# Optimization experiments

Hardware: AMD Instinct MI355X
Metric: run time of the kernel (lower is better)

## Reference

```python
import jax, jax.numpy as jnp
import numpy as np

N = 50000   # nodes
E = 800000  # edges
D = 128     # nfeat == nhid
C = 40      # nclass
L = 4       # nlayer
EPS_BN = 1e-5
EPS_PN = 1e-6
PN_SCALE = 1.0


def setup_inputs() -> dict:
    key = jax.random.key(0)
    ks = jax.random.split(key, 10)
    x = jax.random.normal(ks[0], (N, D), jnp.float32)
    edge_row = jax.random.randint(ks[1], (E,), 0, N)   # destination rows of adj
    edge_col = jax.random.randint(ks[2], (E,), 0, N)   # source cols of adj
    edge_val = jax.random.uniform(ks[3], (E,), jnp.float32)
    # BatchNorm1d(nfeat) affine params
    bn_gamma = jnp.ones((D,), jnp.float32)
    bn_beta = jnp.zeros((D,), jnp.float32)
    s = 1.0 / np.sqrt(D)
    fc_in_w = jax.random.uniform(ks[4], (D, D), jnp.float32, -s, s)
    fc_in_b = jax.random.uniform(ks[5], (D,), jnp.float32, -s, s)
    gc_w = jax.random.uniform(ks[6], (L, D, D), jnp.float32, -s, s)
    gc_b = jax.random.uniform(ks[7], (L, D), jnp.float32, -s, s)
    fc_out_w = jax.random.uniform(ks[8], (D, C), jnp.float32, -s, s)
    fc_out_b = jax.random.uniform(ks[9], (C,), jnp.float32, -s, s)
    return dict(x=x, edge_row=edge_row, edge_col=edge_col, edge_val=edge_val,
                bn_gamma=bn_gamma, bn_beta=bn_beta,
                fc_in_w=fc_in_w, fc_in_b=fc_in_b,
                gc_w=gc_w, gc_b=gc_b,
                fc_out_w=fc_out_w, fc_out_b=fc_out_b)


def pair_norm(x):
    # PairNorm 'PN': center columns, scale by sqrt(mean row squared-norm)
    x = x - x.mean(axis=0, keepdims=True)
    rownorm_mean = jnp.sqrt(EPS_PN + jnp.mean(jnp.sum(x * x, axis=1)))
    return PN_SCALE * x / rownorm_mean


def spmm(edge_row, edge_col, edge_val, h):
    # out[i] = sum_{e: row(e)=i} val_e * h[col(e)]  (torch.spmm(adj, h))
    return jax.ops.segment_sum(edge_val[:, None] * h[edge_col], edge_row, num_segments=N)


def reference(x, edge_row, edge_col, edge_val, bn_gamma, bn_beta,
              fc_in_w, fc_in_b, gc_w, gc_b, fc_out_w, fc_out_b):
    x_old = jnp.zeros_like(x)  # zeros_like(input x), shape [N, D]
    # BatchNorm1d over nodes (batch statistics; dropout inactive / eval)
    mu = x.mean(axis=0)
    var = x.var(axis=0)
    x = (x - mu) / jnp.sqrt(var + EPS_BN) * bn_gamma + bn_beta
    x = x @ fc_in_w + fc_in_b
    for i in range(L):
        h = x @ gc_w[i]                                   # [N, D] dense GEMM
        h = spmm(edge_row, edge_col, edge_val, h) + gc_b[i]
        h = jax.nn.relu(pair_norm(h))
        # skip=1 -> i % 1 == 0 always: residual add every layer
        x = h + x_old
        x_old = x
    return x @ fc_out_w + fc_out_b
```

## Files before the change

### kernel.cpp

```cpp
#include <hip/hip_runtime.h>
#include <hip/hip_bf16.h>


constexpr int DD = 128;

struct alignas(16) f4 { float v[4]; };
typedef unsigned short ushort;
typedef unsigned int uint;
typedef short short8 __attribute__((ext_vector_type(8)));
typedef float f32x4 __attribute__((ext_vector_type(4)));

__device__ inline ushort f2bf(float f) {
    uint u = __float_as_uint(f);
    u += 0x7fffu + ((u >> 16) & 1u);
    return (ushort)(u >> 16);
}

__global__ __launch_bounds__(256) void col_reduce_k(const float* __restrict__ X, int n,
    float* __restrict__ psum, float* __restrict__ psq)
{
    int c = threadIdx.x & (DD - 1);
    int half = threadIdx.x >> 7;
    int rows_per_blk = (n + gridDim.x - 1) / gridDim.x;
    int r0 = blockIdx.x * rows_per_blk;
    int r1 = min(n, r0 + rows_per_blk);
    float s = 0.f, ss = 0.f;
    for (int r = r0 + half; r < r1; r += 2) {
        float v = X[(size_t)r * DD + c];
        s += v; ss += v * v;
    }
    __shared__ float ls[256], lq[256];
    ls[threadIdx.x] = s; lq[threadIdx.x] = ss;
    __syncthreads();
    if (half == 0) {
        psum[blockIdx.x * DD + c] = ls[c] + ls[c + 128];
        psq [blockIdx.x * DD + c] = lq[c] + lq[c + 128];
    }
}

template<bool BN>
__global__ __launch_bounds__(1024) void finalize_k(const float* __restrict__ psum,
    const float* __restrict__ psq, int nblk, int n,
    const float* __restrict__ gamma, const float* __restrict__ beta,
    float* __restrict__ AB)
{
    const int c = threadIdx.x & (DD - 1);
    const int g = threadIdx.x >> 7;
    float s = 0.f, ss = 0.f;
    for (int b = g; b < nblk; b += 8) {
        s  += psum[b * DD + c];
        ss += psq [b * DD + c];
    }
    __shared__ float Ls[8][DD], Lq[8][DD];
    Ls[g][c] = s; Lq[g][c] = ss;
    __syncthreads();
    float ts = 0.f, tss = 0.f;
    #pragma unroll
    for (int k = 0; k < 8; k++) { ts += Ls[k][c]; tss += Lq[k][c]; }
    float mu = ts / (float)n;
    if (BN) {
        if (threadIdx.x < DD) {
            float var = tss / (float)n - mu * mu;
            float a = gamma[c] * rsqrtf(var + 1e-5f);
            AB[c] = a;
            AB[DD + c] = beta[c] - mu * a;
        }
    } else {
        float cent = tss - (float)n * mu * mu;
        __syncthreads();
        if (g == 0) Ls[0][c] = cent;
        __syncthreads();
        for (int off = 64; off > 0; off >>= 1) {
            if (threadIdx.x < off) Ls[0][threadIdx.x] += Ls[0][threadIdx.x + off];
            __syncthreads();
        }
        if (threadIdx.x < DD) {
            float inv = rsqrtf(1e-6f + Ls[0][0] / (float)n);
            AB[c] = inv;
            AB[DD + c] = -mu * inv;
        }
    }
}

__global__ __launch_bounds__(256) void wtrans_k(const float* __restrict__ Wsrc,
    ushort* __restrict__ Wt)
{
    int b = blockIdx.x;
    int w = b >> 4, tile = b & 15;
    int tr = (tile >> 2) * 32, tc = (tile & 3) * 32;
    const float* W = Wsrc + (size_t)w * DD * DD;
    ushort* Wo = Wt + (size_t)w * DD * DD;
    __shared__ float tls[32][33];
    int tx = threadIdx.x & 31, ty = threadIdx.x >> 5;
    #pragma unroll
    for (int j = 0; j < 32; j += 8)
        tls[ty + j][tx] = W[(size_t)(tr + ty + j) * DD + tc + tx];
    __syncthreads();
    #pragma unroll
    for (int j = 0; j < 32; j += 8)
        Wo[(size_t)(tc + ty + j) * DD + (tr + tx)] = f2bf(tls[tx][ty + j]);
}

__global__ __launch_bounds__(256) void wtrans_out_k(const float* __restrict__ W,
    ushort* __restrict__ Wt)
{
    for (int i = threadIdx.x; i < 48 * DD; i += 256) {
        int nn = i >> 7, k = i & 127;
        float v = (nn < 40) ? W[(size_t)k * 40 + nn] : 0.f;
        Wt[i] = f2bf(v);
    }
}

__global__ __launch_bounds__(128) void bias_comp_k(const float* __restrict__ b,
    const float* __restrict__ W0, float* __restrict__ bc)
{
    int nn = threadIdx.x;
    float acc = 0.f;
    for (int j = 0; j < DD; j++) acc += b[j] * W0[(size_t)j * DD + nn];
    bc[nn] = acc;
}

template<int PRE, int NCOLF, int NCOLW, bool BIAS, bool OUTBF, bool WRITEX>
__global__ __launch_bounds__(256) void gemm_mfma_k(const float* __restrict__ IN,
    const ushort* __restrict__ Wt, const float* __restrict__ AB,
    const float* __restrict__ bias, float* __restrict__ Xres,
    void* __restrict__ Yout, int ystride, int n)
{
    __shared__ short xs[64][136];
    __shared__ short ws[NCOLF * 16][136];
    __shared__ float bias_s[DD];
    const int t = threadIdx.x;
    if (BIAS && t < NCOLW) bias_s[t] = bias[t];

    const int row0 = blockIdx.x * 64;
    for (int i = t; i < 64 * 32; i += 256) {
        int m = i >> 5, koff = (i & 31) << 2;
        int r = row0 + m;
        f4 v; v.v[0] = v.v[1] = v.v[2] = v.v[3] = 0.f;
        if (r < n) {
            v = *reinterpret_cast<const f4*>(IN + (size_t)r * DD + koff);
            if (PRE == 1) {
                #pragma unroll
                for (int j = 0; j < 4; j++) v.v[j] = v.v[j] * AB[koff + j] + AB[DD + koff + j];
            } else if (PRE >= 2) {
                #pragma unroll
                for (int j = 0; j < 4; j++)
                    v.v[j] = fmaxf(v.v[j] * AB[koff + j] + AB[DD + koff + j], 0.f);
                if (PRE == 3) {
                    f4 xo = *reinterpret_cast<const f4*>(Xres + (size_t)r * DD + koff);
                    #pragma unroll
                    for (int j = 0; j < 4; j++) v.v[j] += xo.v[j];
                }
            }
            if (WRITEX)
                *reinterpret_cast<f4*>(Xres + (size_t)r * DD + koff) = v;
        }
        uint2 p;
        p.x = (uint)f2bf(v.v[0]) | ((uint)f2bf(v.v[1]) << 16);
        p.y = (uint)f2bf(v.v[2]) | ((uint)f2bf(v.v[3]) << 16);
        *reinterpret_cast<uint2*>(&xs[m][koff]) = p;
    }
    for (int i = t; i < NCOLF * 256; i += 256) {
        int nn = i >> 4, koff = (i & 15) << 3;
        *reinterpret_cast<uint4*>(&ws[nn][koff]) =
            *reinterpret_cast<const uint4*>(Wt + (size_t)nn * DD + koff);
    }
    __syncthreads();

    const int wave = t >> 6, lane = t & 63, fr = lane & 15, g = lane >> 4;
    f32x4 acc[NCOLF];
    #pragma unroll
    for (int c = 0; c < NCOLF; c++) acc[c] = (f32x4){0.f, 0.f, 0.f, 0.f};

    #pragma unroll 2
    for (int ks = 0; ks < 4; ks++) {
        int k0 = ks * 32 + g * 8;
        short8 a = *reinterpret_cast<const short8*>(&xs[wave * 16 + fr][k0]);
        #pragma unroll
        for (int c = 0; c < NCOLF; c++) {
            short8 b = *reinterpret_cast<const short8*>(&ws[c * 16 + fr][k0]);
            acc[c] = __builtin_amdgcn_mfma_f32_16x16x32_bf16(b, a, acc[c], 0, 0, 0);
        }
    }

    const int row = row0 + wave * 16 + fr;
    if (row < n) {
        #pragma unroll
        for (int c = 0; c < NCOLF; c++) {
            int n0 = c * 16 + g * 4;
            if (OUTBF) {
                float b0 = BIAS ? bias_s[n0 + 0] : 0.f, b1 = BIAS ? bias_s[n0 + 1] : 0.f;
                float b2 = BIAS ? bias_s[n0 + 2] : 0.f, b3 = BIAS ? bias_s[n0 + 3] : 0.f;
                uint2 o;
                o.x = (uint)f2bf(acc[c][0] + b0) | ((uint)f2bf(acc[c][1] + b1) << 16);
                o.y = (uint)f2bf(acc[c][2] + b2) | ((uint)f2bf(acc[c][3] + b3) << 16);
                *reinterpret_cast<uint2*>((ushort*)Yout + (size_t)row * DD + n0) = o;
            } else if (n0 + 3 < NCOLW) {
                f4 o;
                #pragma unroll
                for (int j = 0; j < 4; j++)
                    o.v[j] = acc[c][j] + (BIAS ? bias_s[n0 + j] : 0.f);
                *reinterpret_cast<f4*>((float*)Yout + (size_t)row * ystride + n0) = o;
            }
        }
    }
}

__global__ __launch_bounds__(256) void hist_k(const int* __restrict__ erow,
    int* __restrict__ deg, int e)
{
    int i = blockIdx.x * 256 + threadIdx.x;
    if (i < e) atomicAdd(&deg[erow[i]], 1);
}

constexpr int SCAN_TILE = 1024;

__global__ __launch_bounds__(256) void scan1_k(const int* __restrict__ deg,
    int* __restrict__ local, int* __restrict__ bsum, int n)
{
    const int t = threadIdx.x;
    const int base = blockIdx.x * SCAN_TILE + t * 4;
    int v0 = 0, v1 = 0, v2 = 0, v3 = 0;
    if (base + 3 < n) {
        int4 v = *reinterpret_cast<const int4*>(deg + base);
        v0 = v.x; v1 = v.y; v2 = v.z; v3 = v.w;
    } else {
        if (base + 0 < n) v0 = deg[base + 0];
        if (base + 1 < n) v1 = deg[base + 1];
        if (base + 2 < n) v2 = deg[base + 2];
        if (base + 3 < n) v3 = deg[base + 3];
    }
    int s = v0 + v1 + v2 + v3;
    __shared__ int ps[256];
    ps[t] = s;
    __syncthreads();
    for (int off = 1; off < 256; off <<= 1) {
        int add = (t >= off) ? ps[t - off] : 0;
        __syncthreads();
        ps[t] += add;
        __syncthreads();
    }
    int excl = (t > 0) ? ps[t - 1] : 0;
    int o0 = excl, o1 = excl + v0, o2 = o1 + v1, o3 = o2 + v2;
    if (base + 3 < n) {
        int4 o; o.x = o0; o.y = o1; o.z = o2; o.w = o3;
        *reinterpret_cast<int4*>(local + base) = o;
    } else {
        if (base + 0 < n) local[base + 0] = o0;
        if (base + 1 < n) local[base + 1] = o1;
        if (base + 2 < n) local[base + 2] = o2;
        if (base + 3 < n) local[base + 3] = o3;
    }
    if (t == 255) bsum[blockIdx.x] = ps[255];
}

__global__ __launch_bounds__(256) void scan2_k(const int* __restrict__ bsum,
    int* __restrict__ bpre, int nb, int* __restrict__ rowptr, int n)
{
    const int t = threadIdx.x;
    __shared__ int ps[256];
    ps[t] = (t < nb) ? bsum[t] : 0;
    __syncthreads();
    for (int off = 1; off < 256; off <<= 1) {
        int add = (t >= off) ? ps[t - off] : 0;
        __syncthreads();
        ps[t] += add;
        __syncthreads();
    }
    if (t < nb) bpre[t] = (t > 0) ? ps[t - 1] : 0;
    if (t == 255) rowptr[n] = ps[255];
}

__global__ __launch_bounds__(256) void scan3_k(const int* __restrict__ local,
    const int* __restrict__ bpre, int* __restrict__ rowptr, int* __restrict__ cursor, int n)
{
    const int base = blockIdx.x * SCAN_TILE + threadIdx.x * 4;
    const int p = bpre[blockIdx.x];
    if (base + 3 < n) {
        int4 v = *reinterpret_cast<const int4*>(local + base);
        v.x += p; v.y += p; v.z += p; v.w += p;
        *reinterpret_cast<int4*>(rowptr + base) = v;
        *reinterpret_cast<int4*>(cursor + base) = v;
    } else {
        #pragma unroll
        for (int j = 0; j < 4; j++)
            if (base + j < n) {
                int v = local[base + j] + p;
                rowptr[base + j] = v;
                cursor[base + j] = v;
            }
    }
}

__global__ __launch_bounds__(256) void scatter_k(const int* __restrict__ erow,
    const int* __restrict__ ecol, const float* __restrict__ evalv,
    int* __restrict__ cursor, int2* __restrict__ cpair, int e)
{
    int i = blockIdx.x * 256 + threadIdx.x;
    if (i >= e) return;
    int r = erow[i];
    int p = atomicAdd(&cursor[r], 1);
    int2 pr; pr.x = ecol[i]; pr.y = __float_as_int(evalv[i]);
    cpair[p] = pr;
}

__global__ __launch_bounds__(256) void spmm_fused_k(const int* __restrict__ rowptr,
    const int2* __restrict__ cpair, const ushort* __restrict__ H,
    float* __restrict__ AGG, float* __restrict__ psum, float* __restrict__ psq, int n)
{
    const int t = threadIdx.x;
    const int gid = blockIdx.x * 256 + t;
    const int r = gid >> 4;
    const int q = t & 15;
    float a[8];
    #pragma unroll
    for (int j = 0; j < 8; j++) a[j] = 0.f;

    if (r < n) {
        int p0 = rowptr[r], p1 = rowptr[r + 1];
        const ushort* Hq = H + q * 8;
        for (int p = p0; p < p1; p++) {
            int2 cv = cpair[p];
            float v = __int_as_float(cv.y);
            uint4 u = *reinterpret_cast<const uint4*>(Hq + (size_t)cv.x * DD);
            a[0] = fmaf(v, __uint_as_float(u.x << 16), a[0]);
            a[1] = fmaf(v, __uint_as_float(u.x & 0xffff0000u), a[1]);
            a[2] = fmaf(v, __uint_as_float(u.y << 16), a[2]);
            a[3] = fmaf(v, __uint_as_float(u.y & 0xffff0000u), a[3]);
            a[4] = fmaf(v, __uint_as_float(u.z << 16), a[4]);
            a[5] = fmaf(v, __uint_as_float(u.z & 0xffff0000u), a[5]);
            a[6] = fmaf(v, __uint_as_float(u.w << 16), a[6]);
            a[7] = fmaf(v, __uint_as_float(u.w & 0xffff0000u), a[7]);
        }
        float* o = AGG + (size_t)r * DD + q * 8;
        f4 lo; lo.v[0] = a[0]; lo.v[1] = a[1]; lo.v[2] = a[2]; lo.v[3] = a[3];
        f4 hi; hi.v[0] = a[4]; hi.v[1] = a[5]; hi.v[2] = a[6]; hi.v[3] = a[7];
        *reinterpret_cast<f4*>(o) = lo;
        *reinterpret_cast<f4*>(o + 4) = hi;
    }

    float s[8], sq[8];
    #pragma unroll
    for (int j = 0; j < 8; j++) { s[j] = a[j]; sq[j] = a[j] * a[j]; }
    #pragma unroll
    for (int j = 0; j < 8; j++) {
        s[j]  += __shfl_xor(s[j], 16);  sq[j] += __shfl_xor(sq[j], 16);
        s[j]  += __shfl_xor(s[j], 32);  sq[j] += __shfl_xor(sq[j], 32);
    }
    __shared__ float sA[4][DD], qA[4][DD];
    const int wave = t >> 6, lane = t & 63;
    if (lane < 16) {
        #pragma unroll
        for (int j = 0; j < 8; j++) {
            sA[wave][lane * 8 + j] = s[j];
            qA[wave][lane * 8 + j] = sq[j];
        }
    }
    __syncthreads();
    if (t < DD) {
        float S = 0.f, Q = 0.f;
        #pragma unroll
        for (int w = 0; w < 4; w++) { S += sA[w][t]; Q += qA[w][t]; }
        int slot = (blockIdx.x & 63) * DD + t;
        atomicAdd(&psum[slot], S);
        atomicAdd(&psq[slot], Q);
    }
}

extern "C" void kernel_launch(void* const* d_in, const int* in_sizes, int n_in,
                              void* d_out, int out_size, void* d_ws, size_t ws_size,
                              hipStream_t stream)
{
    const float* x_in     = (const float*)d_in[0];
    const int*   erow     = (const int*)d_in[1];
    const int*   ecol     = (const int*)d_in[2];
    const float* evalv    = (const float*)d_in[3];
    const float* gamma    = (const float*)d_in[4];
    const float* beta     = (const float*)d_in[5];
    const float* fc_in_w  = (const float*)d_in[6];
    const float* fc_in_b  = (const float*)d_in[7];
    const float* gc_w     = (const float*)d_in[8];
    const float* fc_out_w = (const float*)d_in[10];
    const float* fc_out_b = (const float*)d_in[11];
    float* out = (float*)d_out;

    const int n = in_sizes[0] / DD;
    const int e = in_sizes[1];
    const int NB = 512;
    const int nscan = (n + SCAN_TILE - 1) / SCAN_TILE;

    char* w = (char*)d_ws;
    float* X      = (float*)w;   w += (size_t)n * DD * 4;
    ushort* Hb    = (ushort*)w;  w += (size_t)n * DD * 2;
    float* AGG    = (float*)w;   w += (size_t)n * DD * 4;
    float* PSUM   = (float*)w;   w += (size_t)NB * DD * 4;
    float* PSQ    = (float*)w;   w += (size_t)NB * DD * 4;
    float* PSUMS  = (float*)w;   w += (size_t)64 * DD * 4;
    float* PSQS   = (float*)w;   w += (size_t)64 * DD * 4;
    float* AB     = (float*)w;   w += 2 * DD * 4;
    ushort* Wt    = (ushort*)w;  w += (size_t)4 * DD * DD * 2;
    ushort* Wtc   = (ushort*)w;  w += (size_t)DD * DD * 2;
    ushort* WtO   = (ushort*)w;  w += (size_t)48 * DD * 2;
    float* Ycomp  = (float*)w;   w += (size_t)DD * DD * 4;
    float* bc     = (float*)w;   w += DD * 4;
    int* deg      = (int*)w;     w += (size_t)(n + 4) * 4;
    int* rowptr   = (int*)w;     w += (size_t)(n + 4) * 4;
    int* cursor   = (int*)w;     w += (size_t)(n + 4) * 4;
    int* slocal   = (int*)w;     w += (size_t)(n + 4) * 4;
    int* bsum     = (int*)w;     w += 1024;
    int* bpre     = (int*)w;     w += 1024;
    int2* cpair   = (int2*)w;    w += (size_t)e * 8;

    hipMemsetAsync(deg, 0, (size_t)n * 4, stream);
    hist_k<<<(e + 255) / 256, 256, 0, stream>>>(erow, deg, e);
    scan1_k<<<nscan, 256, 0, stream>>>(deg, slocal, bsum, n);
    scan2_k<<<1, 256, 0, stream>>>(bsum, bpre, nscan, rowptr, n);
    scan3_k<<<nscan, 256, 0, stream>>>(slocal, bpre, rowptr, cursor, n);
    scatter_k<<<(e + 255) / 256, 256, 0, stream>>>(erow, ecol, evalv, cursor, cpair, e);

    wtrans_k<<<64, 256, 0, stream>>>(gc_w, Wt);
    gemm_mfma_k<0, 8, 128, false, false, false><<<2, 256, 0, stream>>>(
        fc_in_w, Wt, nullptr, nullptr, nullptr, Ycomp, DD, DD);
    wtrans_k<<<16, 256, 0, stream>>>(Ycomp, Wtc);
    bias_comp_k<<<1, 128, 0, stream>>>(fc_in_b, gc_w, bc);
    wtrans_out_k<<<1, 256, 0, stream>>>(fc_out_w, WtO);

    col_reduce_k<<<NB, 256, 0, stream>>>(x_in, n, PSUM, PSQ);
    finalize_k<true><<<1, 1024, 0, stream>>>(PSUM, PSQ, NB, n, gamma, beta, AB);

    const int gblocks64 = (n + 63) / 64;
    const int sblocks = ((size_t)n * 16 + 255) / 256;

    gemm_mfma_k<1, 8, 128, true, true, false><<<gblocks64, 256, 0, stream>>>(
        x_in, Wtc, AB, bc, nullptr, Hb, DD, n);

    for (int l = 0; l < 4; l++) {
        hipMemsetAsync(PSUMS, 0, (size_t)2 * 64 * DD * 4, stream);
        spmm_fused_k<<<sblocks, 256, 0, stream>>>(rowptr, cpair, Hb, AGG, PSUMS, PSQS, n);
        finalize_k<false><<<1, 1024, 0, stream>>>(PSUMS, PSQS, 64, n, nullptr, nullptr, AB);
        if (l < 3) {
            if (l == 0)
                gemm_mfma_k<2, 8, 128, false, true, true><<<gblocks64, 256, 0, stream>>>(
                    AGG, Wt + (size_t)(l + 1) * DD * DD, AB, nullptr, X, Hb, DD, n);
            else
                gemm_mfma_k<3, 8, 128, false, true, true><<<gblocks64, 256, 0, stream>>>(
                    AGG, Wt + (size_t)(l + 1) * DD * DD, AB, nullptr, X, Hb, DD, n);
        } else {
            gemm_mfma_k<3, 3, 40, true, false, false><<<gblocks64, 256, 0, stream>>>(
                AGG, WtO, AB, fc_out_b, X, out, 40, n);
        }
    }
}
```

Baseline: 444.9 us.

## Store activations in bf16 and build CSR via two-pass bucketed binning

```diff
diff --git a/kernel.cpp b/kernel.cpp
--- a/kernel.cpp
+++ b/kernel.cpp
@@ -14,6 +14,20 @@
     uint u = __float_as_uint(f);
     u += 0x7fffu + ((u >> 16) & 1u);
     return (ushort)(u >> 16);
+}
+__device__ inline void bf8_unpack(uint4 u, float* v) {
+    v[0] = __uint_as_float(u.x << 16); v[1] = __uint_as_float(u.x & 0xffff0000u);
+    v[2] = __uint_as_float(u.y << 16); v[3] = __uint_as_float(u.y & 0xffff0000u);
+    v[4] = __uint_as_float(u.z << 16); v[5] = __uint_as_float(u.z & 0xffff0000u);
+    v[6] = __uint_as_float(u.w << 16); v[7] = __uint_as_float(u.w & 0xffff0000u);
+}
+__device__ inline uint4 bf8_pack(const float* v) {
+    uint4 o;
+    o.x = (uint)f2bf(v[0]) | ((uint)f2bf(v[1]) << 16);
+    o.y = (uint)f2bf(v[2]) | ((uint)f2bf(v[3]) << 16);
+    o.z = (uint)f2bf(v[4]) | ((uint)f2bf(v[5]) << 16);
+    o.w = (uint)f2bf(v[6]) | ((uint)f2bf(v[7]) << 16);
+    return o;
 }
 
 __global__ __launch_bounds__(256) void col_reduce_k(const float* __restrict__ X, int n,
@@ -121,9 +135,9 @@
 }
 
 template<int PRE, int NCOLF, int NCOLW, bool BIAS, bool OUTBF, bool WRITEX>
-__global__ __launch_bounds__(256) void gemm_mfma_k(const float* __restrict__ IN,
+__global__ __launch_bounds__(256) void gemm_mfma_k(const void* __restrict__ INv,
     const ushort* __restrict__ Wt, const float* __restrict__ AB,
-    const float* __restrict__ bias, float* __restrict__ Xres,
+    const float* __restrict__ bias, void* __restrict__ Xresv,
     void* __restrict__ Yout, int ystride, int n)
 {
     __shared__ short xs[64][136];
@@ -133,32 +147,52 @@
     if (BIAS && t < NCOLW) bias_s[t] = bias[t];
 
     const int row0 = blockIdx.x * 64;
-    for (int i = t; i < 64 * 32; i += 256) {
-        int m = i >> 5, koff = (i & 31) << 2;
-        int r = row0 + m;
-        f4 v; v.v[0] = v.v[1] = v.v[2] = v.v[3] = 0.f;
-        if (r < n) {
-            v = *reinterpret_cast<const f4*>(IN + (size_t)r * DD + koff);
-            if (PRE == 1) {
-                #pragma unroll
-                for (int j = 0; j < 4; j++) v.v[j] = v.v[j] * AB[koff + j] + AB[DD + koff + j];
-            } else if (PRE >= 2) {
-                #pragma unroll
-                for (int j = 0; j < 4; j++)
-                    v.v[j] = fmaxf(v.v[j] * AB[koff + j] + AB[DD + koff + j], 0.f);
-                if (PRE == 3) {
-                    f4 xo = *reinterpret_cast<const f4*>(Xres + (size_t)r * DD + koff);
+    if (PRE <= 1) {
+        const float* IN = (const float*)INv;
+        for (int i = t; i < 64 * 32; i += 256) {
+            int m = i >> 5, koff = (i & 31) << 2;
+            int r = row0 + m;
+            f4 v; v.v[0] = v.v[1] = v.v[2] = v.v[3] = 0.f;
+            if (r < n) {
+                v = *reinterpret_cast<const f4*>(IN + (size_t)r * DD + koff);
+                if (PRE == 1) {
                     #pragma unroll
-                    for (int j = 0; j < 4; j++) v.v[j] += xo.v[j];
+                    for (int j = 0; j < 4; j++) v.v[j] = v.v[j] * AB[koff + j] + AB[DD + koff + j];
                 }
             }
-            if (WRITEX)
-                *reinterpret_cast<f4*>(Xres + (size_t)r * DD + koff) = v;
-        }
-        uint2 p;
-        p.x = (uint)f2bf(v.v[0]) | ((uint)f2bf(v.v[1]) << 16);
-        p.y = (uint)f2bf(v.v[2]) | ((uint)f2bf(v.v[3]) << 16);
-        *reinterpret_cast<uint2*>(&xs[m][koff]) = p;
+            uint2 p;
+            p.x = (uint)f2bf(v.v[0]) | ((uint)f2bf(v.v[1]) << 16);
+            p.y = (uint)f2bf(v.v[2]) | ((uint)f2bf(v.v[3]) << 16);
+            *reinterpret_cast<uint2*>(&xs[m][koff]) = p;
+        }
+    } else {
+        const ushort* IN = (const ushort*)INv;
+        ushort* Xres = (ushort*)Xresv;
+        for (int i = t; i < 64 * 16; i += 256) {
+            int m = i >> 4, k8 = (i & 15) << 3;
+            int r = row0 + m;
+            float v[8];
+            if (r < n) {
+                uint4 u = *reinterpret_cast<const uint4*>(IN + (size_t)r * DD + k8);
+                bf8_unpack(u, v);
+                #pragma unroll
+                for (int j = 0; j < 8; j++)
+                    v[j] = fmaxf(v[j] * AB[k8 + j] + AB[DD + k8 + j], 0.f);
+                if (PRE == 3) {
+                    uint4 xo = *reinterpret_cast<const uint4*>(Xres + (size_t)r * DD + k8);
+                    float xov[8]; bf8_unpack(xo, xov);
+                    #pragma unroll
+                    for (int j = 0; j < 8; j++) v[j] += xov[j];
+                }
+                uint4 pk = bf8_pack(v);
+                if (WRITEX)
+                    *reinterpret_cast<uint4*>(Xres + (size_t)r * DD + k8) = pk;
+                *reinterpret_cast<uint4*>(&xs[m][k8]) = pk;
+            } else {
+                uint4 z; z.x = z.y = z.z = z.w = 0u;
+                *reinterpret_cast<uint4*>(&xs[m][k8]) = z;
+            }
+        }
     }
     for (int i = t; i < NCOLF * 256; i += 256) {
         int nn = i >> 4, koff = (i & 15) << 3;
@@ -214,6 +248,7 @@
 }
 
 constexpr int SCAN_TILE = 1024;
+constexpr int BSH = 9;
 
 __global__ __launch_bounds__(256) void scan1_k(const int* __restrict__ deg,
     int* __restrict__ local, int* __restrict__ bsum, int n)
@@ -292,21 +327,68 @@
     }
 }
 
-__global__ __launch_bounds__(256) void scatter_k(const int* __restrict__ erow,
+__global__ void gcur_init_k(const int* __restrict__ rowptr, int* __restrict__ gcur,
+    int n, int nbuk)
+{
+    int b = threadIdx.x;
+    if (b <= nbuk) gcur[b] = rowptr[min(b << BSH, n)];
+}
+
+__global__ __launch_bounds__(256) void bin_a_k(const int* __restrict__ erow,
     const int* __restrict__ ecol, const float* __restrict__ evalv,
-    int* __restrict__ cursor, int2* __restrict__ cpair, int e)
-{
-    int i = blockIdx.x * 256 + threadIdx.x;
-    if (i >= e) return;
-    int r = erow[i];
-    int p = atomicAdd(&cursor[r], 1);
-    int2 pr; pr.x = ecol[i]; pr.y = __float_as_int(evalv[i]);
-    cpair[p] = pr;
+    int* __restrict__ gcur, uint2* __restrict__ binned, int e)
+{
+    __shared__ int cnt[128];
+    __shared__ int base[128];
+    const int t = threadIdx.x;
+    if (t < 128) cnt[t] = 0;
+    __syncthreads();
+    const int i0 = blockIdx.x * 2048 + t * 8;
+    int rw[8], cl[8], rk[8];
+    float vl[8];
+    #pragma unroll
+    for (int j = 0; j < 8; j++) {
+        int idx = i0 + j;
+        if (idx < e) { rw[j] = erow[idx]; cl[j] = ecol[idx]; vl[j] = evalv[idx]; }
+        else rw[j] = -1;
+    }
+    #pragma unroll
+    for (int j = 0; j < 8; j++)
+        if (rw[j] >= 0) rk[j] = atomicAdd(&cnt[rw[j] >> BSH], 1);
+    __syncthreads();
+    if (t < 128) base[t] = cnt[t] ? atomicAdd(&gcur[t], cnt[t]) : 0;
+    __syncthreads();
+    #pragma unroll
+    for (int j = 0; j < 8; j++) {
+        if (rw[j] >= 0) {
+            int b = rw[j] >> BSH, rl = rw[j] & ((1 << BSH) - 1);
+            uint2 pr;
+            pr.x = (uint)cl[j] | ((uint)rl << 16);
+            pr.y = __float_as_uint(vl[j]);
+            binned[base[b] + rk[j]] = pr;
+        }
+    }
+}
+
+__global__ __launch_bounds__(256) void bin_b_k(const uint2* __restrict__ binned,
+    const int* __restrict__ rowptr, int* __restrict__ cursor,
+    int2* __restrict__ cpair, int n)
+{
+    const int b = blockIdx.x;
+    const int r0 = min(b << BSH, n), r1 = min((b + 1) << BSH, n);
+    const int p0 = rowptr[r0], p1 = rowptr[r1];
+    for (int p = p0 + threadIdx.x; p < p1; p += 256) {
+        uint2 u = binned[p];
+        int r = (b << BSH) + (int)(u.x >> 16);
+        int pos = atomicAdd(&cursor[r], 1);
+        int2 pr; pr.x = (int)(u.x & 0xffffu); pr.y = (int)u.y;
+        cpair[pos] = pr;
+    }
 }
 
 __global__ __launch_bounds__(256) void spmm_fused_k(const int* __restrict__ rowptr,
     const int2* __restrict__ cpair, const ushort* __restrict__ H,
-    float* __restrict__ AGG, float* __restrict__ psum, float* __restrict__ psq, int n)
+    ushort* __restrict__ AGG, float* __restrict__ psum, float* __restrict__ psq, int n)
 {
     const int t = threadIdx.x;
     const int gid = blockIdx.x * 256 + t;
@@ -332,11 +414,7 @@
             a[6] = fmaf(v, __uint_as_float(u.w << 16), a[6]);
             a[7] = fmaf(v, __uint_as_float(u.w & 0xffff0000u), a[7]);
         }
-        float* o = AGG + (size_t)r * DD + q * 8;
-        f4 lo; lo.v[0] = a[0]; lo.v[1] = a[1]; lo.v[2] = a[2]; lo.v[3] = a[3];
-        f4 hi; hi.v[0] = a[4]; hi.v[1] = a[5]; hi.v[2] = a[6]; hi.v[3] = a[7];
-        *reinterpret_cast<f4*>(o) = lo;
-        *reinterpret_cast<f4*>(o + 4) = hi;
+        *reinterpret_cast<uint4*>(AGG + (size_t)r * DD + q * 8) = bf8_pack(a);
     }
 
     float s[8], sq[8];
@@ -388,11 +466,12 @@
     const int e = in_sizes[1];
     const int NB = 512;
     const int nscan = (n + SCAN_TILE - 1) / SCAN_TILE;
+    const int nbuk = (n + (1 << BSH) - 1) >> BSH;
 
     char* w = (char*)d_ws;
-    float* X      = (float*)w;   w += (size_t)n * DD * 4;
+    ushort* X     = (ushort*)w;  w += (size_t)n * DD * 2;
     ushort* Hb    = (ushort*)w;  w += (size_t)n * DD * 2;
-    float* AGG    = (float*)w;   w += (size_t)n * DD * 4;
+    ushort* AGG   = (ushort*)w;  w += (size_t)n * DD * 2;
     float* PSUM   = (float*)w;   w += (size_t)NB * DD * 4;
     float* PSQ    = (float*)w;   w += (size_t)NB * DD * 4;
     float* PSUMS  = (float*)w;   w += (size_t)64 * DD * 4;
@@ -409,6 +488,8 @@
     int* slocal   = (int*)w;     w += (size_t)(n + 4) * 4;
     int* bsum     = (int*)w;     w += 1024;
     int* bpre     = (int*)w;     w += 1024;
+    int* gcur     = (int*)w;     w += 1024;
+    uint2* binned = (uint2*)w;   w += (size_t)e * 8;
     int2* cpair   = (int2*)w;    w += (size_t)e * 8;
 
     hipMemsetAsync(deg, 0, (size_t)n * 4, stream);
@@ -416,7 +497,9 @@
     scan1_k<<<nscan, 256, 0, stream>>>(deg, slocal, bsum, n);
     scan2_k<<<1, 256, 0, stream>>>(bsum, bpre, nscan, rowptr, n);
     scan3_k<<<nscan, 256, 0, stream>>>(slocal, bpre, rowptr, cursor, n);
-    scatter_k<<<(e + 255) / 256, 256, 0, stream>>>(erow, ecol, evalv, cursor, cpair, e);
+    gcur_init_k<<<1, 128, 0, stream>>>(rowptr, gcur, n, nbuk);
+    bin_a_k<<<(e + 2047) / 2048, 256, 0, stream>>>(erow, ecol, evalv, gcur, binned, e);
+    bin_b_k<<<nbuk, 256, 0, stream>>>(binned, rowptr, cursor, cpair, n);
 
     wtrans_k<<<64, 256, 0, stream>>>(gc_w, Wt);
     gemm_mfma_k<0, 8, 128, false, false, false><<<2, 256, 0, stream>>>(
```

New measurement: 419.2 us. 1.06x faster.
